# Performance work log

Measured on AMD Instinct MI355X. Metric: run time of the kernel, lower is better.

The kernel has to match this reference:

```python
import jax, jax.numpy as jnp
import numpy as np

N = 50000      # nodes
E = 800000     # edges
D = 128        # node_feat_dim
ED = 64        # edge_feat_dim
C = 10         # num_fine_classes
BN_EPS = 1e-5


def _lin(key, fan_in, fan_out):
    k1, k2 = jax.random.split(key)
    s = 1.0 / np.sqrt(fan_in)
    W = jax.random.uniform(k1, (fan_in, fan_out), jnp.float32, -s, s)
    b = jax.random.uniform(k2, (fan_out,), jnp.float32, -s, s)
    return W, b


def setup_inputs() -> dict:
    key = jax.random.key(0)
    ks = jax.random.split(key, 16)
    nfeats = jax.random.normal(ks[0], (N, D), jnp.float32)
    efeats = jax.random.normal(ks[1], (E, ED), jnp.float32)
    src = jax.random.randint(ks[2], (E,), 0, N, jnp.int64 if jax.config.jax_enable_x64 else jnp.int32)
    dst = jax.random.randint(ks[3], (E,), 0, N, src.dtype)
    # SAGE layer 1 and 2 (E-GraphSAGE style)
    Wm1, bm1 = _lin(ks[4], D + ED, D)   # W_msg: cat(h_src, e) -> D
    Wa1, ba1 = _lin(ks[5], 2 * D, D)    # W_apply: cat(h, h_neigh) -> D
    Wm2, bm2 = _lin(ks[6], D + ED, D)
    Wa2, ba2 = _lin(ks[7], 2 * D, D)
    # coarse head: Linear(2D,32) -> ReLU -> Linear(32,2)
    Wc1, bc1 = _lin(ks[8], 2 * D, 32)
    Wc2, bc2 = _lin(ks[9], 32, 2)
    # fine head: Linear(2D,64) -> BN(64) -> ReLU -> Dropout(eval) -> Linear(64,C)
    Wf1, bf1 = _lin(ks[10], 2 * D, 64)
    bn_g = jnp.ones((64,), jnp.float32)
    bn_b = jnp.zeros((64,), jnp.float32)
    bn_m = jax.random.normal(ks[11], (64,), jnp.float32) * 0.1
    bn_v = jax.random.uniform(ks[12], (64,), jnp.float32, 0.5, 1.5)
    Wf2, bf2 = _lin(ks[13], 64, C)
    return dict(nfeats=nfeats, efeats=efeats, src=src, dst=dst,
                Wm1=Wm1, bm1=bm1, Wa1=Wa1, ba1=ba1,
                Wm2=Wm2, bm2=bm2, Wa2=Wa2, ba2=ba2,
                Wc1=Wc1, bc1=bc1, Wc2=Wc2, bc2=bc2,
                Wf1=Wf1, bf1=bf1, bn_g=bn_g, bn_b=bn_b, bn_m=bn_m, bn_v=bn_v,
                Wf2=Wf2, bf2=bf2)


def _sage_layer(h, efeats, src, dst, Wm, bm, Wa, ba):
    # per-edge message from source node + edge feature
    m = jnp.concatenate([h[src], efeats], axis=1) @ Wm + bm        # [E, D]
    # mean-aggregate messages onto destination nodes
    summed = jax.ops.segment_sum(m, dst, num_segments=N)            # [N, D]
    deg = jax.ops.segment_sum(jnp.ones((E, 1), h.dtype), dst, num_segments=N)
    h_neigh = summed / jnp.maximum(deg, 1.0)
    return jax.nn.leaky_relu(jnp.concatenate([h, h_neigh], axis=1) @ Wa + ba, 0.01)


def reference(nfeats, efeats, src, dst,
              Wm1, bm1, Wa1, ba1, Wm2, bm2, Wa2, ba2,
              Wc1, bc1, Wc2, bc2,
              Wf1, bf1, bn_g, bn_b, bn_m, bn_v, Wf2, bf2):
    h = _sage_layer(nfeats, efeats, src, dst, Wm1, bm1, Wa1, ba1)
    h = _sage_layer(h, efeats, src, dst, Wm2, bm2, Wa2, ba2)  # dropout is identity in eval
    pair = jnp.concatenate([h[src], h[dst]], axis=1)           # [E, 2D]
    coarse = jax.nn.relu(pair @ Wc1 + bc1) @ Wc2 + bc2         # [E, 2]
    x = pair @ Wf1 + bf1
    x = bn_g * (x - bn_m) * jax.lax.rsqrt(bn_v + BN_EPS) + bn_b  # eval-mode BatchNorm1d
    fine = jax.nn.relu(x) @ Wf2 + bf2                            # [E, C]
    return coarse, fine
```

## Files before the change

kernel.cpp:

```cpp
#include <hip/hip_runtime.h>

#define N_NODES 50000
#define N_EDGES 800000
#define SCAN_NBLK 196

typedef unsigned int uint;
typedef unsigned short ushort;
typedef __attribute__((ext_vector_type(4))) float f32x4;
typedef __attribute__((ext_vector_type(2))) float f32x2;
typedef __attribute__((ext_vector_type(8))) short s16x8;
typedef __attribute__((ext_vector_type(4))) uint u32x4;

__device__ __forceinline__ float bf2f(uint lo16) { return __uint_as_float(lo16 << 16); }
__device__ __forceinline__ ushort f2bf(float f) {
    uint u = __float_as_uint(f);
    u = u + 0x7fffu + ((u >> 16) & 1u);
    return (ushort)(u >> 16);
}
__device__ __forceinline__ bool is_bf16(const uint* tag) { return *tag != 0x3F800000u; }
__device__ __forceinline__ float ldf(const void* p, long i, bool bf) {
    return bf ? bf2f(((const ushort*)p)[i]) : ((const float*)p)[i];
}

__global__ __launch_bounds__(256) void k_prep(
    const void* Wm1, const void* Wa1, const void* Wm2, const void* Wa2,
    const void* Wc1, const void* Wf1,
    ushort* wA1, ushort* wB1, ushort* wa1, ushort* wA2, ushort* wB2, ushort* wa2, ushort* wPF,
    const void* bc1, const void* wc2, const void* bc2,
    const void* bf1, const void* g, const void* bb, const void* m, const void* v,
    const void* wf2, const void* bf2,
    const void* bm1, const void* ba1, const void* bm2, const void* ba2,
    float* __restrict__ pp, int* __restrict__ cur, const uint* __restrict__ tag)
{
    const bool bf = is_bf16(tag);
    int gidx = blockIdx.x * 256 + threadIdx.x;
    if (gidx < N_NODES) cur[gidx] = 0;

    if (blockIdx.x == 544) {
        int t = threadIdx.x; const int T = 256;
        for (int i = t; i < 32; i += T) pp[i] = ldf(bc1, i, bf);
        for (int i = t; i < 64; i += T) pp[32 + i] = ldf(wc2, i, bf);
        for (int i = t; i < 2;  i += T) pp[96 + i] = ldf(bc2, i, bf);
        for (int i = t; i < 64; i += T) {
            float s_ = ldf(g, i, bf) * rsqrtf(ldf(v, i, bf) + 1e-5f);
            pp[98 + i]  = s_;
            pp[162 + i] = (ldf(bf1, i, bf) - ldf(m, i, bf)) * s_ + ldf(bb, i, bf);
        }
        for (int i = t; i < 640; i += T) pp[226 + i] = ldf(wf2, i, bf);
        for (int i = t; i < 10;  i += T) pp[866 + i] = ldf(bf2, i, bf);
        for (int i = t; i < 128; i += T) {
            pp[876 + i]  = ldf(bm1, i, bf);
            pp[1004 + i] = ldf(ba1, i, bf);
            pp[1132 + i] = ldf(bm2, i, bf);
            pp[1260 + i] = ldf(ba2, i, bf);
        }
        return;
    }

    int idx = gidx;
#define SEG(SZ, Wp, LDW, RO, KC, Dp) \
    if (idx < (SZ)) { int n_ = idx / (KC), k_ = idx & ((KC) - 1); \
        (Dp)[n_ * (KC) + k_] = f2bf(ldf((Wp), (long)((RO) + k_) * (LDW) + n_, bf)); return; } \
    idx -= (SZ);
    SEG(16384, Wm1, 128, 0,   128, wA1)
    SEG(8192,  Wm1, 128, 128, 64,  wB1)
    SEG(32768, Wa1, 128, 0,   256, wa1)
    SEG(16384, Wm2, 128, 0,   128, wA2)
    SEG(8192,  Wm2, 128, 128, 64,  wB2)
    SEG(32768, Wa2, 128, 0,   256, wa2)
    SEG(4096,  Wc1, 32,  0,   128, wPF)
    SEG(4096,  Wc1, 32,  128, 128, wPF + 32 * 128)
    SEG(8192,  Wf1, 64,  0,   128, wPF + 64 * 128)
    SEG(8192,  Wf1, 64,  128, 128, wPF + 128 * 128)
#undef SEG
}

__global__ void k_count(const int* __restrict__ dst, int* __restrict__ cnt) {
    int e = blockIdx.x * 256 + threadIdx.x;
    if (e < N_EDGES) atomicAdd(&cnt[dst[e]], 1);
}

__global__ __launch_bounds__(256) void k_scan1(const int* __restrict__ cnt,
                                               int* __restrict__ rs, int* __restrict__ bsum)
{
    __shared__ int sh[256];
    int tid = threadIdx.x;
    int n = blockIdx.x * 256 + tid;
    int c = (n < N_NODES) ? cnt[n] : 0;
    sh[tid] = c;
    __syncthreads();
    #pragma unroll
    for (int off = 1; off < 256; off <<= 1) {
        int v = (tid >= off) ? sh[tid - off] : 0;
        __syncthreads();
        sh[tid] += v;
        __syncthreads();
    }
    if (n < N_NODES) rs[n] = sh[tid] - c;
    if (tid == 255) bsum[blockIdx.x] = sh[255];
}

__global__ __launch_bounds__(256) void k_scan2(const int* __restrict__ bsum,
                                               int* __restrict__ boff, int* __restrict__ rs)
{
    __shared__ int sh[256];
    int tid = threadIdx.x;
    int v = (tid < SCAN_NBLK) ? bsum[tid] : 0;
    sh[tid] = v;
    __syncthreads();
    #pragma unroll
    for (int off = 1; off < 256; off <<= 1) {
        int u = (tid >= off) ? sh[tid - off] : 0;
        __syncthreads();
        sh[tid] += u;
        __syncthreads();
    }
    if (tid < SCAN_NBLK) boff[tid] = sh[tid] - v;
    if (tid == 255) rs[N_NODES] = sh[255];
}

__global__ __launch_bounds__(256) void k_scan3(int* __restrict__ rs, const int* __restrict__ boff,
                                               int* __restrict__ cur)
{
    int n = blockIdx.x * 256 + threadIdx.x;
    if (n < N_NODES) {
        int v = rs[n] + boff[blockIdx.x];
        rs[n] = v;
        cur[n] = v;
    }
}

__global__ void k_fill(const int* __restrict__ dst, const int* __restrict__ src,
                       int* __restrict__ cur, int* __restrict__ eidx, int* __restrict__ ssrc) {
    int e = blockIdx.x * 256 + threadIdx.x;
    if (e < N_EDGES) {
        int p = atomicAdd(&cur[dst[e]], 1);
        eidx[p] = e;
        ssrc[p] = src[e];
    }
}

__global__ __launch_bounds__(256) void k_sef(
    const void* __restrict__ ef, const int* __restrict__ rs, const int* __restrict__ eix,
    float* __restrict__ sef, const uint* __restrict__ tag)
{
    bool bf = is_bf16(tag);
    int n = blockIdx.x * 4 + (threadIdx.x >> 6);
    if (n >= N_NODES) return;
    int lane = threadIdx.x & 63;
    int s0 = rs[n], s1 = rs[n + 1];
    if (bf) {
        int g = lane >> 3, l = lane & 7;
        const ushort* efp = (const ushort*)ef;
        float acc[8] = {};
        for (int base = s0; base < s1; base += 64) {
            int cnt = s1 - base; if (cnt > 64) cnt = 64;
            int pre = (base + lane < s1) ? eix[base + lane] : 0;
            int T = (cnt + 7) >> 3;
            for (int t = 0; t < T; t += 2) {
                int j0 = g + t * 8;
                int j1 = j0 + 8;
                long e0 = __shfl(pre, j0, 64);
                long e1 = __shfl(pre, j1 & 63, 64);
                if (j0 < cnt) {
                    u32x4 u0 = *(const u32x4*)(efp + e0 * 64 + l * 8);
                    #pragma unroll
                    for (int q = 0; q < 4; q++) {
                        acc[2 * q]     += bf2f(u0[q] & 0xffffu);
                        acc[2 * q + 1] += bf2f(u0[q] >> 16);
                    }
                }
                if (j1 < cnt) {
                    u32x4 u1 = *(const u32x4*)(efp + e1 * 64 + l * 8);
                    #pragma unroll
                    for (int q = 0; q < 4; q++) {
                        acc[2 * q]     += bf2f(u1[q] & 0xffffu);
                        acc[2 * q + 1] += bf2f(u1[q] >> 16);
                    }
                }
            }
        }
        #pragma unroll
        for (int m = 0; m < 8; m++) {
            acc[m] += __shfl_xor(acc[m], 8, 64);
            acc[m] += __shfl_xor(acc[m], 16, 64);
            acc[m] += __shfl_xor(acc[m], 32, 64);
        }
        if (g == 0) {
            *(f32x4*)&sef[(long)n * 64 + l * 8]     = f32x4{acc[0], acc[1], acc[2], acc[3]};
            *(f32x4*)&sef[(long)n * 64 + l * 8 + 4] = f32x4{acc[4], acc[5], acc[6], acc[7]};
        }
    } else {
        int g = lane >> 4, l = lane & 15;
        const float* efp = (const float*)ef;
        f32x4 acc = {0.f, 0.f, 0.f, 0.f};
        for (int base = s0; base < s1; base += 64) {
            int cnt = s1 - base; if (cnt > 64) cnt = 64;
            int pre = (base + lane < s1) ? eix[base + lane] : 0;
            int T = (cnt + 3) >> 2;
            for (int t = 0; t < T; t += 2) {
                int j0 = g + t * 4;
                int j1 = j0 + 4;
                long e0 = __shfl(pre, j0, 64);
                long e1 = __shfl(pre, j1 & 63, 64);
                if (j0 < cnt) acc += *(const f32x4*)(efp + e0 * 64 + l * 4);
                if (j1 < cnt) acc += *(const f32x4*)(efp + e1 * 64 + l * 4);
            }
        }
        #pragma unroll
        for (int m = 0; m < 4; m++) {
            acc[m] += __shfl_xor(acc[m], 16, 64);
            acc[m] += __shfl_xor(acc[m], 32, 64);
        }
        if (g == 0) *(f32x4*)&sef[(long)n * 64 + l * 4] = acc;
    }
}

template<int K1, int NOUT, int EPI>
__device__ __forceinline__ void gemm_body(ushort* xs,
    const void* __restrict__ X1, int dt1,
    const ushort* __restrict__ Wt,
    void* __restrict__ Y, int M, bool bf, int mblk)
{
    constexpr int K = K1;
    constexpr int KT = K / 32;
    constexpr int NT = NOUT / 16;
    constexpr int PITCH = K + 8;
    constexpr int KP = K / 2;
    const int m0 = mblk * 64;
    const int tid = threadIdx.x;

    for (int idx = tid; idx < 64 * KP; idx += 256) {
        int r = idx / KP, kp = idx - r * KP;
        int row = m0 + r;
        uint val = 0u;
        if (row < M) {
            long base = (long)row * K1 + kp * 2;
            bool f32src = (dt1 == 2) || (dt1 == 1 && !bf);
            if (f32src) {
                const float* fp = (const float*)X1;
                val = (uint)f2bf(fp[base]) | ((uint)f2bf(fp[base + 1]) << 16);
            } else {
                val = ((const uint*)X1)[base >> 1];
            }
        }
        *(uint*)&xs[r * PITCH + kp * 2] = val;
    }
    __syncthreads();

    const int lane = tid & 63, wid = tid >> 6;
    const int l16 = lane & 15, lh = lane >> 4;

    s16x8 afr[KT];
    const ushort* xrow = &xs[(wid * 16 + l16) * PITCH + lh * 8];
    #pragma unroll
    for (int ks = 0; ks < KT; ks++) afr[ks] = *(const s16x8*)(xrow + ks * 32);

    f32x4 acc[NT] = {};
    #pragma unroll
    for (int nt = 0; nt < NT; nt++) {
        const ushort* wrow = &Wt[(long)(nt * 16 + l16) * K + lh * 8];
        #pragma unroll
        for (int ks = 0; ks < KT; ks++) {
            s16x8 bfr = *(const s16x8*)(wrow + ks * 32);
            acc[nt] = __builtin_amdgcn_mfma_f32_16x16x32_bf16(afr[ks], bfr, acc[nt], 0, 0, 0);
        }
    }

    #pragma unroll
    for (int nt = 0; nt < NT; nt++) {
        int col = nt * 16 + l16;
        #pragma unroll
        for (int r = 0; r < 4; r++) {
            int row = m0 + wid * 16 + lh * 4 + r;
            if (row < M) {
                float v = acc[nt][r];
                if (EPI == 2) ((float*)Y)[(long)row * NOUT + col] = v;
                else          ((ushort*)Y)[(long)row * NOUT + col] = f2bf(v);
            }
        }
    }
}

__global__ __launch_bounds__(256) void k_fatAB(
    const void* __restrict__ XA, int dtA, const ushort* __restrict__ wA, ushort* __restrict__ A,
    const float* __restrict__ sef, const ushort* __restrict__ wB, float* __restrict__ SB,
    int nA, const uint* __restrict__ tag)
{
    __shared__ ushort xs[64 * 136];
    bool bf = is_bf16(tag);
    if ((int)blockIdx.x < nA)
        gemm_body<128, 128, 0>(xs, XA, dtA, wA, A, N_NODES, bf, blockIdx.x);
    else
        gemm_body<64, 128, 2>(xs, sef, 2, wB, SB, N_NODES, bf, blockIdx.x - nA);
}

__global__ __launch_bounds__(256) void k_agg(
    const ushort* __restrict__ A, const float* __restrict__ SB,
    const int* __restrict__ rs, const int* __restrict__ ssrc,
    const float* __restrict__ bm, ushort* __restrict__ hn)
{
    int n = blockIdx.x * 4 + (threadIdx.x >> 6);
    if (n >= N_NODES) return;
    int lane = threadIdx.x & 63;
    int g = lane >> 4, l = lane & 15;
    int s0 = rs[n], s1 = rs[n + 1];
    float acc[8] = {};
    for (int base = s0; base < s1; base += 64) {
        int cnt = s1 - base; if (cnt > 64) cnt = 64;
        int pre = (base + lane < s1) ? ssrc[base + lane] : 0;
        int T = (cnt + 3) >> 2;
        for (int t = 0; t < T; t += 2) {
            int j0 = g + t * 4;
            int j1 = j0 + 4;
            long i0 = __shfl(pre, j0, 64);
            long i1 = __shfl(pre, j1 & 63, 64);
            if (j0 < cnt) {
                u32x4 u0 = *(const u32x4*)&A[i0 * 128 + l * 8];
                #pragma unroll
                for (int q = 0; q < 4; q++) {
                    acc[2 * q]     += bf2f(u0[q] & 0xffffu);
                    acc[2 * q + 1] += bf2f(u0[q] >> 16);
                }
            }
            if (j1 < cnt) {
                u32x4 u1 = *(const u32x4*)&A[i1 * 128 + l * 8];
                #pragma unroll
                for (int q = 0; q < 4; q++) {
                    acc[2 * q]     += bf2f(u1[q] & 0xffffu);
                    acc[2 * q + 1] += bf2f(u1[q] >> 16);
                }
            }
        }
    }
    #pragma unroll
    for (int m = 0; m < 8; m++) {
        acc[m] += __shfl_xor(acc[m], 16, 64);
        acc[m] += __shfl_xor(acc[m], 32, 64);
    }
    if (g == 0) {
        int deg = s1 - s0;
        u32x4 ov = {0u, 0u, 0u, 0u};
        if (deg > 0) {
            float inv = 1.f / (float)deg;
            f32x4 sb0 = *(const f32x4*)&SB[(long)n * 128 + l * 8];
            f32x4 sb1 = *(const f32x4*)&SB[(long)n * 128 + l * 8 + 4];
            float h[8];
            #pragma unroll
            for (int m = 0; m < 8; m++) {
                float sbv = (m < 4) ? sb0[m] : sb1[m - 4];
                h[m] = (acc[m] + sbv) * inv + bm[l * 8 + m];
            }
            #pragma unroll
            for (int q = 0; q < 4; q++)
                ov[q] = (uint)f2bf(h[2 * q]) | ((uint)f2bf(h[2 * q + 1]) << 16);
        }
        *(u32x4*)&hn[(long)n * 128 + l * 8] = ov;
    }
}

template<int LAYER2>
__global__ __launch_bounds__(256) void k_apply(
    const void* __restrict__ X1, int dt1, const ushort* __restrict__ hn,
    const ushort* __restrict__ Wt, const float* __restrict__ bias,
    ushort* __restrict__ Hout,
    const ushort* __restrict__ wPF, ushort* __restrict__ PFs, ushort* __restrict__ PFd,
    const uint* __restrict__ tag)
{
    constexpr int PITCH = 264;
    __shared__ ushort xs[64 * PITCH];
    __shared__ ushort ys[LAYER2 ? 64 * 136 : 1];
    const bool bf = is_bf16(tag);
    const int m0 = blockIdx.x * 64;
    const int tid = threadIdx.x;
    const int lane = tid & 63, wid = tid >> 6;

    for (int idx = tid; idx < 64 * 128; idx += 256) {
        int r = idx >> 7, kp = idx & 127;
        int row = m0 + r;
        uint val = 0u;
        if (row < N_NODES) {
            if (kp < 64) {
                long base = (long)row * 128 + kp * 2;
                if (dt1 == 1 && !bf) {
                    const float* fp = (const float*)X1;
                    val = (uint)f2bf(fp[base]) | ((uint)f2bf(fp[base + 1]) << 16);
                } else {
                    val = ((const uint*)X1)[base >> 1];
                }
            } else {
                val = ((const uint*)hn)[((long)row * 128 + (kp - 64) * 2) >> 1];
            }
        }
        *(uint*)&xs[r * PITCH + kp * 2] = val;
    }
    __syncthreads();

    const int l16 = lane & 15, lh = lane >> 4;

    s16x8 afr[8];
    const ushort* xrow = &xs[(wid * 16 + l16) * PITCH + lh * 8];
    #pragma unroll
    for (int ks = 0; ks < 8; ks++) afr[ks] = *(const s16x8*)(xrow + ks * 32);

    f32x4 acc[8] = {};
    #pragma unroll
    for (int nt = 0; nt < 8; nt++) {
        const ushort* wrow = &Wt[(long)(nt * 16 + l16) * 256 + lh * 8];
        #pragma unroll
        for (int ks = 0; ks < 8; ks++) {
            s16x8 bfr = *(const s16x8*)(wrow + ks * 32);
            acc[nt] = __builtin_amdgcn_mfma_f32_16x16x32_bf16(afr[ks], bfr, acc[nt], 0, 0, 0);
        }
    }

    #pragma unroll
    for (int nt = 0; nt < 8; nt++) {
        int col = nt * 16 + l16;
        float bv = bias[col];
        #pragma unroll
        for (int r = 0; r < 4; r++) {
            int rl = wid * 16 + lh * 4 + r;
            int row = m0 + rl;
            float v = acc[nt][r] + bv;
            v = v > 0.f ? v : 0.01f * v;
            if (LAYER2) {
                ys[rl * 136 + col] = f2bf(v);
            } else if (row < N_NODES) {
                Hout[(long)row * 128 + col] = f2bf(v);
            }
        }
    }

    if (LAYER2) {
        __syncthreads();
        s16x8 af2[4];
        const ushort* yrow = &ys[(wid * 16 + l16) * 136 + lh * 8];
        #pragma unroll
        for (int ks = 0; ks < 4; ks++) af2[ks] = *(const s16x8*)(yrow + ks * 32);

        f32x4 ac2[12] = {};
        #pragma unroll
        for (int nt = 0; nt < 12; nt++) {
            const ushort* wrow = &wPF[(long)(nt * 16 + l16) * 128 + lh * 8];
            #pragma unroll
            for (int ks = 0; ks < 4; ks++) {
                s16x8 bfr = *(const s16x8*)(wrow + ks * 32);
                ac2[nt] = __builtin_amdgcn_mfma_f32_16x16x32_bf16(af2[ks], bfr, ac2[nt], 0, 0, 0);
            }
        }
        #pragma unroll
        for (int nt = 0; nt < 12; nt++) {
            int col = nt * 16 + l16;
            ushort* T; int c2;
            if (col < 64) { T = (col < 32) ? PFs : PFd; c2 = col & 31; }
            else if (col < 128) { T = PFs; c2 = col - 32; }
            else                { T = PFd; c2 = col - 96; }
            #pragma unroll
            for (int r = 0; r < 4; r++) {
                int row = m0 + wid * 16 + lh * 4 + r;
                if (row < N_NODES)
                    T[(long)row * 128 + c2] = f2bf(ac2[nt][r]);
            }
        }
    }
}

__global__ __launch_bounds__(256) void k_head(
    const ushort* __restrict__ PFs, const ushort* __restrict__ PFd,
    const int* __restrict__ src, const int* __restrict__ dst,
    const float* __restrict__ pp, void* __restrict__ out, const uint* __restrict__ tag)
{
    __shared__ float sp[876];
    for (int i = threadIdx.x; i < 876; i += 256) sp[i] = pp[i];
    __syncthreads();
    const float* bc1 = sp;        const float* wc2 = sp + 32;  const float* bc2 = sp + 96;
    const float* sbn = sp + 98;   const float* tbn = sp + 162;
    const float* wf2 = sp + 226;  const float* bf2 = sp + 866;
    bool bf = is_bf16(tag);
    int e = blockIdx.x * 256 + threadIdx.x;
    if (e >= N_EDGES) return;
    int s = src[e], d = dst[e];
    const ushort* ps = PFs + (long)s * 128;
    const ushort* pd = PFd + (long)d * 128;

    float c0 = bc2[0], c1 = bc2[1];
    #pragma unroll
    for (int jb = 0; jb < 32; jb += 8) {
        u32x4 ua = *(const u32x4*)(ps + jb);
        u32x4 ub = *(const u32x4*)(pd + jb);
        #pragma unroll
        for (int q = 0; q < 4; q++) {
            int j = jb + q * 2;
            float p0 = bf2f(ua[q] & 0xffffu) + bf2f(ub[q] & 0xffffu) + bc1[j];
            float p1 = bf2f(ua[q] >> 16)     + bf2f(ub[q] >> 16)     + bc1[j + 1];
            p0 = fmaxf(p0, 0.f);
            p1 = fmaxf(p1, 0.f);
            c0 += p0 * wc2[j * 2 + 0] + p1 * wc2[j * 2 + 2];
            c1 += p0 * wc2[j * 2 + 1] + p1 * wc2[j * 2 + 3];
        }
    }

    float fa[10];
    #pragma unroll
    for (int j = 0; j < 10; j++) fa[j] = bf2[j];
    #pragma unroll
    for (int db = 0; db < 64; db += 8) {
        u32x4 ua = *(const u32x4*)(ps + 32 + db);
        u32x4 ub = *(const u32x4*)(pd + 32 + db);
        #pragma unroll
        for (int q = 0; q < 4; q++) {
            int dd = db + q * 2;
            float x0 = (bf2f(ua[q] & 0xffffu) + bf2f(ub[q] & 0xffffu)) * sbn[dd] + tbn[dd];
            float x1 = (bf2f(ua[q] >> 16)     + bf2f(ub[q] >> 16))     * sbn[dd + 1] + tbn[dd + 1];
            x0 = fmaxf(x0, 0.f);
            x1 = fmaxf(x1, 0.f);
            #pragma unroll
            for (int j = 0; j < 10; j++)
                fa[j] += x0 * wf2[dd * 10 + j] + x1 * wf2[(dd + 1) * 10 + j];
        }
    }

    if (bf) {
        uint* oc = (uint*)out;
        oc[e] = (uint)f2bf(c0) | ((uint)f2bf(c1) << 16);
        uint* of = (uint*)((ushort*)out + 2L * N_EDGES + 10L * e);
        #pragma unroll
        for (int j = 0; j < 5; j++)
            of[j] = (uint)f2bf(fa[2 * j]) | ((uint)f2bf(fa[2 * j + 1]) << 16);
    } else {
        float* o = (float*)out;
        *(f32x2*)&o[2L * e] = f32x2{c0, c1};
        float* of = o + 2L * N_EDGES + 10L * e;
        #pragma unroll
        for (int j = 0; j < 5; j++)
            *(f32x2*)&of[2 * j] = f32x2{fa[2 * j], fa[2 * j + 1]};
    }
}

extern "C" void kernel_launch(void* const* d_in, const int* in_sizes, int n_in,
                              void* d_out, int out_size, void* d_ws, size_t ws_size,
                              hipStream_t stream)
{
    (void)in_sizes; (void)n_in; (void)out_size; (void)ws_size;
    const void* nf  = d_in[0];
    const void* ef  = d_in[1];
    const int* src  = (const int*)d_in[2];
    const int* dst  = (const int*)d_in[3];
    const void* Wm1 = d_in[4];  const void* bm1 = d_in[5];
    const void* Wa1 = d_in[6];  const void* ba1 = d_in[7];
    const void* Wm2 = d_in[8];  const void* bm2 = d_in[9];
    const void* Wa2 = d_in[10]; const void* ba2 = d_in[11];
    const void* Wc1 = d_in[12]; const void* bc1 = d_in[13];
    const void* Wc2 = d_in[14]; const void* bc2 = d_in[15];
    const void* Wf1 = d_in[16]; const void* bf1 = d_in[17];
    const void* bng = d_in[18]; const void* bnb = d_in[19];
    const void* bnm = d_in[20]; const void* bnv = d_in[21];
    const void* Wf2 = d_in[22]; const void* bf2 = d_in[23];
    const uint* tag = (const uint*)d_in[18];

    char* w = (char*)d_ws;
    size_t o = 0;
    auto alloc = [&](size_t b) -> char* { char* p = w + o; o += (b + 255) & ~(size_t)255; return p; };
    ushort* wA1 = (ushort*)alloc(128 * 128 * 2);
    ushort* wB1 = (ushort*)alloc(128 * 64 * 2);
    ushort* wa1 = (ushort*)alloc(128 * 256 * 2);
    ushort* wA2 = (ushort*)alloc(128 * 128 * 2);
    ushort* wB2 = (ushort*)alloc(128 * 64 * 2);
    ushort* wa2 = (ushort*)alloc(128 * 256 * 2);
    ushort* wPF = (ushort*)alloc(192 * 128 * 2);
    float*  pp  = (float*)alloc(1388 * 4);
    int*    rs  = (int*)alloc((N_NODES + 1) * 4);
    int*    cur = (int*)alloc(N_NODES * 4);
    int*    bsum = (int*)alloc(SCAN_NBLK * 4);
    int*    boff = (int*)alloc(SCAN_NBLK * 4);
    int*    eix = (int*)alloc((size_t)N_EDGES * 4);
    int*    ssr = (int*)alloc((size_t)N_EDGES * 4);
    float*  sef = (float*)alloc((size_t)N_NODES * 64 * 4);
    float*  SBb = (float*)alloc((size_t)N_NODES * 128 * 4);
    ushort* A   = (ushort*)alloc((size_t)N_NODES * 128 * 2);
    ushort* hn  = (ushort*)alloc((size_t)N_NODES * 128 * 2);
    ushort* h1  = (ushort*)alloc((size_t)N_NODES * 128 * 2);
    ushort* PFs = (ushort*)alloc((size_t)N_NODES * 128 * 2);
    ushort* PFd = (ushort*)alloc((size_t)N_NODES * 128 * 2);

    const int GB_N = (N_NODES + 63) / 64;
    const int EB   = N_EDGES / 256;
    const int NB4  = (N_NODES + 3) / 4;

    k_prep<<<545, 256, 0, stream>>>(Wm1, Wa1, Wm2, Wa2, Wc1, Wf1,
                                    wA1, wB1, wa1, wA2, wB2, wa2, wPF,
                                    bc1, Wc2, bc2, bf1, bng, bnb, bnm, bnv, Wf2, bf2,
                                    bm1, ba1, bm2, ba2, pp, cur, tag);
    k_count<<<EB, 256, 0, stream>>>(dst, cur);
    k_scan1<<<SCAN_NBLK, 256, 0, stream>>>(cur, rs, bsum);
    k_scan2<<<1, 256, 0, stream>>>(bsum, boff, rs);
    k_scan3<<<SCAN_NBLK, 256, 0, stream>>>(rs, boff, cur);
    k_fill<<<EB, 256, 0, stream>>>(dst, src, cur, eix, ssr);
    k_sef<<<NB4, 256, 0, stream>>>(ef, rs, eix, sef, tag);

    k_fatAB<<<2 * GB_N, 256, 0, stream>>>(nf, 1, wA1, A, sef, wB1, SBb, GB_N, tag);
    k_agg<<<NB4, 256, 0, stream>>>(A, SBb, rs, ssr, pp + 876, hn);
    k_apply<0><<<GB_N, 256, 0, stream>>>(nf, 1, hn, wa1, pp + 1004, h1,
                                         nullptr, nullptr, nullptr, tag);

    k_fatAB<<<2 * GB_N, 256, 0, stream>>>(h1, 0, wA2, A, sef, wB2, SBb, GB_N, tag);
    k_agg<<<NB4, 256, 0, stream>>>(A, SBb, rs, ssr, pp + 1132, hn);
    k_apply<1><<<GB_N, 256, 0, stream>>>(h1, 0, hn, wa2, pp + 1260, nullptr,
                                         wPF, PFs, PFd, tag);

    k_head<<<EB, 256, 0, stream>>>(PFs, PFd, src, dst, pp, d_out, tag);
}
```

Measured before the change: 483.9 us.

## Fuse layer-2 source GEMM into layer-1 apply and merge scan kernels

Layer-1 apply now also multiplies its output tile by the layer-2 message weight and writes A directly, so the separate layer-2 source GEMM launch and the extra read of h1 go away. Both layers' edge-feature GEMMs run in one launch into separate SB buffers. The second and third scan kernels are merged so each block rescans the block sums itself. The aggregation loop is unrolled to four gathers per iteration. In exchange the layer-1 apply uses more shared memory and registers, and an extra SB buffer is allocated.

```diff
diff --git a/kernel.cpp b/kernel.cpp
--- a/kernel.cpp
+++ b/kernel.cpp
@@ -100,8 +100,8 @@
     if (tid == 255) bsum[blockIdx.x] = sh[255];
 }
 
-__global__ __launch_bounds__(256) void k_scan2(const int* __restrict__ bsum,
-                                               int* __restrict__ boff, int* __restrict__ rs)
+__global__ __launch_bounds__(256) void k_scan23(const int* __restrict__ bsum,
+                                                int* __restrict__ rs, int* __restrict__ cur)
 {
     __shared__ int sh[256];
     int tid = threadIdx.x;
@@ -115,19 +115,14 @@
         sh[tid] += u;
         __syncthreads();
     }
-    if (tid < SCAN_NBLK) boff[tid] = sh[tid] - v;
-    if (tid == 255) rs[N_NODES] = sh[255];
-}
-
-__global__ __launch_bounds__(256) void k_scan3(int* __restrict__ rs, const int* __restrict__ boff,
-                                               int* __restrict__ cur)
-{
-    int n = blockIdx.x * 256 + threadIdx.x;
+    int boff = (blockIdx.x == 0) ? 0 : sh[blockIdx.x - 1];
+    int n = blockIdx.x * 256 + tid;
     if (n < N_NODES) {
-        int v = rs[n] + boff[blockIdx.x];
-        rs[n] = v;
-        cur[n] = v;
-    }
+        int r = rs[n] + boff;
+        rs[n] = r;
+        cur[n] = r;
+    }
+    if (blockIdx.x == 0 && tid == 0) rs[N_NODES] = sh[SCAN_NBLK - 1];
 }
 
 __global__ void k_fill(const int* __restrict__ dst, const int* __restrict__ src,
@@ -282,17 +277,22 @@
     }
 }
 
-__global__ __launch_bounds__(256) void k_fatAB(
+__global__ __launch_bounds__(256) void k_fat3(
     const void* __restrict__ XA, int dtA, const ushort* __restrict__ wA, ushort* __restrict__ A,
-    const float* __restrict__ sef, const ushort* __restrict__ wB, float* __restrict__ SB,
+    const float* __restrict__ sef,
+    const ushort* __restrict__ wB1, float* __restrict__ SB1,
+    const ushort* __restrict__ wB2, float* __restrict__ SB2,
     int nA, const uint* __restrict__ tag)
 {
     __shared__ ushort xs[64 * 136];
     bool bf = is_bf16(tag);
-    if ((int)blockIdx.x < nA)
-        gemm_body<128, 128, 0>(xs, XA, dtA, wA, A, N_NODES, bf, blockIdx.x);
+    int b = blockIdx.x;
+    if (b < nA)
+        gemm_body<128, 128, 0>(xs, XA, dtA, wA, A, N_NODES, bf, b);
+    else if (b < 2 * nA)
+        gemm_body<64, 128, 2>(xs, sef, 2, wB1, SB1, N_NODES, bf, b - nA);
     else
-        gemm_body<64, 128, 2>(xs, sef, 2, wB, SB, N_NODES, bf, blockIdx.x - nA);
+        gemm_body<64, 128, 2>(xs, sef, 2, wB2, SB2, N_NODES, bf, b - 2 * nA);
 }
 
 __global__ __launch_bounds__(256) void k_agg(
@@ -310,25 +310,43 @@
         int cnt = s1 - base; if (cnt > 64) cnt = 64;
         int pre = (base + lane < s1) ? ssrc[base + lane] : 0;
         int T = (cnt + 3) >> 2;
-        for (int t = 0; t < T; t += 2) {
+        for (int t = 0; t < T; t += 4) {
             int j0 = g + t * 4;
-            int j1 = j0 + 4;
+            int j1 = j0 + 4, j2 = j0 + 8, j3 = j0 + 12;
             long i0 = __shfl(pre, j0, 64);
             long i1 = __shfl(pre, j1 & 63, 64);
+            long i2 = __shfl(pre, j2 & 63, 64);
+            long i3 = __shfl(pre, j3 & 63, 64);
             if (j0 < cnt) {
-                u32x4 u0 = *(const u32x4*)&A[i0 * 128 + l * 8];
+                u32x4 u = *(const u32x4*)&A[i0 * 128 + l * 8];
                 #pragma unroll
                 for (int q = 0; q < 4; q++) {
-                    acc[2 * q]     += bf2f(u0[q] & 0xffffu);
-                    acc[2 * q + 1] += bf2f(u0[q] >> 16);
+                    acc[2 * q]     += bf2f(u[q] & 0xffffu);
+                    acc[2 * q + 1] += bf2f(u[q] >> 16);
                 }
             }
             if (j1 < cnt) {
-                u32x4 u1 = *(const u32x4*)&A[i1 * 128 + l * 8];
+                u32x4 u = *(const u32x4*)&A[i1 * 128 + l * 8];
                 #pragma unroll
                 for (int q = 0; q < 4; q++) {
-                    acc[2 * q]     += bf2f(u1[q] & 0xffffu);
-                    acc[2 * q + 1] += bf2f(u1[q] >> 16);
+                    acc[2 * q]     += bf2f(u[q] & 0xffffu);
+                    acc[2 * q + 1] += bf2f(u[q] >> 16);
+                }
+            }
+            if (j2 < cnt) {
+                u32x4 u = *(const u32x4*)&A[i2 * 128 + l * 8];
+                #pragma unroll
+                for (int q = 0; q < 4; q++) {
+                    acc[2 * q]     += bf2f(u[q] & 0xffffu);
+                    acc[2 * q + 1] += bf2f(u[q] >> 16);
+                }
+            }
+            if (j3 < cnt) {
+                u32x4 u = *(const u32x4*)&A[i3 * 128 + l * 8];
+                #pragma unroll
+                for (int q = 0; q < 4; q++) {
+                    acc[2 * q]     += bf2f(u[q] & 0xffffu);
+                    acc[2 * q + 1] += bf2f(u[q] >> 16);
                 }
             }
         }
@@ -359,17 +377,18 @@
     }
 }
 
-template<int LAYER2>
+template<int MODE>
 __global__ __launch_bounds__(256) void k_apply(
     const void* __restrict__ X1, int dt1, const ushort* __restrict__ hn,
     const ushort* __restrict__ Wt, const float* __restrict__ bias,
     ushort* __restrict__ Hout,
-    const ushort* __restrict__ wPF, ushort* __restrict__ PFs, ushort* __restrict__ PFd,
+    const ushort* __restrict__ Wt2, ushort* __restrict__ Y2a, ushort* __restrict__ Y2b,
     const uint* __restrict__ tag)
 {
     constexpr int PITCH = 264;
+    constexpr int NT2 = MODE ? 12 : 8;
     __shared__ ushort xs[64 * PITCH];
-    __shared__ ushort ys[LAYER2 ? 64 * 136 : 1];
+    __shared__ ushort ys[64 * 136];
     const bool bf = is_bf16(tag);
     const int m0 = blockIdx.x * 64;
     const int tid = threadIdx.x;
@@ -424,44 +443,45 @@
             int row = m0 + rl;
             float v = acc[nt][r] + bv;
             v = v > 0.f ? v : 0.01f * v;
-            if (LAYER2) {
-                ys[rl * 136 + col] = f2bf(v);
-            } else if (row < N_NODES) {
-                Hout[(long)row * 128 + col] = f2bf(v);
-            }
-        }
-    }
-
-    if (LAYER2) {
-        __syncthreads();
-        s16x8 af2[4];
-        const ushort* yrow = &ys[(wid * 16 + l16) * 136 + lh * 8];
-        #pragma unroll
-        for (int ks = 0; ks < 4; ks++) af2[ks] = *(const s16x8*)(yrow + ks * 32);
-
-        f32x4 ac2[12] = {};
-        #pragma unroll
-        for (int nt = 0; nt < 12; nt++) {
-            const ushort* wrow = &wPF[(long)(nt * 16 + l16) * 128 + lh * 8];
-            #pragma unroll
-            for (int ks = 0; ks < 4; ks++) {
-                s16x8 bfr = *(const s16x8*)(wrow + ks * 32);
-                ac2[nt] = __builtin_amdgcn_mfma_f32_16x16x32_bf16(af2[ks], bfr, ac2[nt], 0, 0, 0);
-            }
-        }
-        #pragma unroll
-        for (int nt = 0; nt < 12; nt++) {
-            int col = nt * 16 + l16;
-            ushort* T; int c2;
-            if (col < 64) { T = (col < 32) ? PFs : PFd; c2 = col & 31; }
-            else if (col < 128) { T = PFs; c2 = col - 32; }
-            else                { T = PFd; c2 = col - 96; }
-            #pragma unroll
-            for (int r = 0; r < 4; r++) {
-                int row = m0 + wid * 16 + lh * 4 + r;
-                if (row < N_NODES)
-                    T[(long)row * 128 + c2] = f2bf(ac2[nt][r]);
-            }
+            ushort hv = f2bf(v);
+            ys[rl * 136 + col] = hv;
+            if (MODE == 0 && row < N_NODES)
+                Hout[(long)row * 128 + col] = hv;
+        }
+    }
+    __syncthreads();
+
+    s16x8 af2[4];
+    const ushort* yrow = &ys[(wid * 16 + l16) * 136 + lh * 8];
+    #pragma unroll
+    for (int ks = 0; ks < 4; ks++) af2[ks] = *(const s16x8*)(yrow + ks * 32);
+
+    f32x4 ac2[NT2] = {};
+    #pragma unroll
+    for (int nt = 0; nt < NT2; nt++) {
+        const ushort* wrow = &Wt2[(long)(nt * 16 + l16) * 128 + lh * 8];
+        #pragma unroll
+        for (int ks = 0; ks < 4; ks++) {
+            s16x8 bfr = *(const s16x8*)(wrow + ks * 32);
+            ac2[nt] = __builtin_amdgcn_mfma_f32_16x16x32_bf16(af2[ks], bfr, ac2[nt], 0, 0, 0);
+        }
+    }
+    #pragma unroll
+    for (int nt = 0; nt < NT2; nt++) {
+        int col = nt * 16 + l16;
+        ushort* T; int c2;
+        if (MODE == 0) {
+            T = Y2a; c2 = col;
+        } else {
+            if (col < 64) { T = (col < 32) ? Y2a : Y2b; c2 = col & 31; }
+            else if (col < 128) { T = Y2a; c2 = col - 32; }
+            else                { T = Y2b; c2 = col - 96; }
+        }
+        #pragma unroll
+        for (int r = 0; r < 4; r++) {
+            int row = m0 + wid * 16 + lh * 4 + r;
+            if (row < N_NODES)
+                T[(long)row * 128 + c2] = f2bf(ac2[nt][r]);
         }
     }
 }
@@ -573,11 +593,11 @@
     int*    rs  = (int*)alloc((N_NODES + 1) * 4);
     int*    cur = (int*)alloc(N_NODES * 4);
     int*    bsum = (int*)alloc(SCAN_NBLK * 4);
-    int*    boff = (int*)alloc(SCAN_NBLK * 4);
     int*    eix = (int*)alloc((size_t)N_EDGES * 4);
     int*    ssr = (int*)alloc((size_t)N_EDGES * 4);
     float*  sef = (float*)alloc((size_t)N_NODES * 64 * 4);
-    float*  SBb = (float*)alloc((size_t)N_NODES * 128 * 4);
+    float*  SB1 = (float*)alloc((size_t)N_NODES * 128 * 4);
+    float*  SB2 = (float*)alloc((size_t)N_NODES * 128 * 4);
     ushort* A   = (ushort*)alloc((size_t)N_NODES * 128 * 2);
     ushort* hn  = (ushort*)alloc((size_t)N_NODES * 128 * 2);
     ushort* h1  = (ushort*)alloc((size_t)N_NODES * 128 * 2);
@@ -594,18 +614,17 @@
                                     bm1, ba1, bm2, ba2, pp, cur, tag);
     k_count<<<EB, 256, 0, stream>>>(dst, cur);
     k_scan1<<<SCAN_NBLK, 256, 0, stream>>>(cur, rs, bsum);
-    k_scan2<<<1, 256, 0, stream>>>(bsum, boff, rs);
-    k_scan3<<<SCAN_NBLK, 256, 0, stream>>>(rs, boff, cur);
+    k_scan23<<<SCAN_NBLK, 256, 0, stream>>>(bsum, rs, cur);
     k_fill<<<EB, 256, 0, stream>>>(dst, src, cur, eix, ssr);
     k_sef<<<NB4, 256, 0, stream>>>(ef, rs, eix, sef, tag);
 
-    k_fatAB<<<2 * GB_N, 256, 0, stream>>>(nf, 1, wA1, A, sef, wB1, SBb, GB_N, tag);
-    k_agg<<<NB4, 256, 0, stream>>>(A, SBb, rs, ssr, pp + 876, hn);
+    k_fat3<<<3 * GB_N, 256, 0, stream>>>(nf, 1, wA1, A, sef, wB1, SB1, wB2, SB2, GB_N, tag);
+
+    k_agg<<<NB4, 256, 0, stream>>>(A, SB1, rs, ssr, pp + 876, hn);
     k_apply<0><<<GB_N, 256, 0, stream>>>(nf, 1, hn, wa1, pp + 1004, h1,
-                                         nullptr, nullptr, nullptr, tag);
-
-    k_fatAB<<<2 * GB_N, 256, 0, stream>>>(h1, 0, wA2, A, sef, wB2, SBb, GB_N, tag);
-    k_agg<<<NB4, 256, 0, stream>>>(A, SBb, rs, ssr, pp + 1132, hn);
+                                         wA2, A, nullptr, tag);
+
+    k_agg<<<NB4, 256, 0, stream>>>(A, SB2, rs, ssr, pp + 1132, hn);
     k_apply<1><<<GB_N, 256, 0, stream>>>(h1, 0, hn, wa2, pp + 1260, nullptr,
                                          wPF, PFs, PFd, tag);
 
```

Result: no change. 480.9 us (-0.6%).
